# Performance work log

Hardware: AMD Instinct MI355X
Metric: run time of the kernel (lower is better)

## Reference

```python
import jax, jax.numpy as jnp
import numpy as np
import math

N, C_S, C_Z, C_IPA, H, NQ, NV = 768, 384, 128, 16, 12, 4, 8


def setup_inputs() -> dict:
    key = jax.random.key(0)
    ks = jax.random.split(key, 16)
    inp = {
        "s": jax.random.normal(ks[0], (N, C_S), jnp.float32),
        "z": jax.random.normal(ks[1], (N, N, C_Z), jnp.float32),
        "rots": jax.random.normal(ks[2], (N, 3, 3), jnp.float32),
        "trans": jax.random.normal(ks[3], (N, 3), jnp.float32),
        "mask": jnp.ones((N,), jnp.float32),
    }
    sc = 0.02
    inp["Wq"] = jax.random.normal(ks[4], (C_S, H * C_IPA), jnp.float32) * sc
    inp["bq"] = jnp.zeros((H * C_IPA,), jnp.float32)
    inp["Wkv"] = jax.random.normal(ks[5], (C_S, H * 2 * C_IPA), jnp.float32) * sc
    inp["bkv"] = jnp.zeros((H * 2 * C_IPA,), jnp.float32)
    inp["Wq3"] = jax.random.normal(ks[6], (C_S, H * 3 * NQ), jnp.float32) * sc
    inp["bq3"] = jnp.zeros((H * 3 * NQ,), jnp.float32)
    inp["Wkv3"] = jax.random.normal(ks[7], (C_S, H * 3 * (NQ + NV)), jnp.float32) * sc
    inp["bkv3"] = jnp.zeros((H * 3 * (NQ + NV),), jnp.float32)
    inp["Wb"] = jax.random.normal(ks[8], (C_Z, H), jnp.float32) * sc
    inp["bb"] = jnp.zeros((H,), jnp.float32)
    inp["hw"] = jnp.zeros((H,), jnp.float32)
    inp["Wo"] = jax.random.normal(ks[9], (H * (C_Z + C_IPA + NV * 4), C_S), jnp.float32) * sc
    inp["bo"] = jnp.zeros((C_S,), jnp.float32)
    return inp


def reference(s, z, rots, trans, mask, Wq, bq, Wkv, bkv, Wq3, bq3, Wkv3, bkv3, Wb, bb, hw, Wo, bo):
    normsize = math.sqrt(1.0 / (3 * C_IPA))
    normsize_B = math.sqrt(1.0 / 3.0)
    normsize_hw = math.sqrt(1.0 / (3 * NQ * 9.0 / 2))

    # scalar Q/K/V: [N, H, C_IPA]
    Q = (s @ Wq + bq).reshape(N, H, C_IPA)
    KV = (s @ Wkv + bkv).reshape(N, H, 2, C_IPA)
    K, V = KV[..., 0, :], KV[..., 1, :]

    # query points: project, place into global frame via rigid transform
    Q3 = (s @ Wq3 + bq3).reshape(N, 3, NQ * H).swapaxes(-1, -2)        # [N, NQ*H, 3]
    Q3 = jnp.einsum('nij,nkj->nki', rots, Q3) + trans[:, None, :]
    Q3 = Q3.reshape(N, H, NQ, 3)

    KV3 = (s @ Wkv3 + bkv3).reshape(N, 3, H * (NQ + NV)).swapaxes(-1, -2)
    KV3 = jnp.einsum('nij,nkj->nki', rots, KV3) + trans[:, None, :]
    KV3 = KV3.reshape(N, H, NQ + NV, 3)
    K3, V3 = KV3[:, :, :NQ, :], KV3[:, :, NQ:, :]                      # points per head

    # pair bias [N, N, H]
    B = z @ Wb + bb

    # scalar attention logits + pair bias
    AT = jnp.einsum('ihc,jhc->ijh', Q, K) * normsize + B * normsize_B

    # point attention: squared distances [N, N, H, NQ]
    d2 = jnp.sum(jnp.square(Q3[:, None] - K3[None, :]), axis=-1)
    hw_sp = jax.nn.softplus(hw) * normsize_hw                          # [H]
    AT3 = -0.5 * jnp.sum(d2 * hw_sp[None, None, :, None], axis=-1)     # [N, N, H]

    # mask bias: large negative where either residue masked out
    mask2 = mask[:, None] * mask[None, :]
    B3 = (mask2 - 1.0) * 1e9                                           # [N, N]

    AT = jax.nn.softmax(AT + AT3 + B3[..., None], axis=-2)             # softmax over j

    # scalar value aggregation
    O = jnp.einsum('ijh,jhc->ihc', AT, V).reshape(N, -1)

    # point value aggregation, then map back to local frame (inverse transform)
    O3 = jnp.einsum('ijh,jhcd->ihcd', AT, V3).reshape(N, H * NV, 3)
    O3 = jnp.einsum('nji,nkj->nki', rots, O3 - trans[:, None, :])      # rots^T @ (O3 - t)
    O3_norm = jnp.sqrt(jnp.sum(jnp.square(O3), axis=-1) + 1e-20)       # [N, H*NV]

    # pair representation aggregation
    O_pair = jnp.einsum('ijh,ijc->ihc', AT, z).reshape(N, -1)

    O_final = jnp.concatenate((O, O3[..., 0], O3[..., 1], O3[..., 2], O3_norm, O_pair), axis=-1)
    return O_final @ Wo + bo
```

## Files before the change

kernel.cpp:

```cpp
#include <hip/hip_runtime.h>
#include <cstdint>


typedef __attribute__((ext_vector_type(8))) short short8;
typedef __attribute__((ext_vector_type(4))) short short4_t;
typedef __attribute__((ext_vector_type(4))) float f32x4;

__device__ __forceinline__ unsigned short f2bf(float f) {
    unsigned u = __float_as_uint(f);
    u = (u + 0x7FFFu + ((u >> 16) & 1u)) >> 16;
    return (unsigned short)u;
}
__device__ __forceinline__ float bf2f(unsigned short s) {
    return __uint_as_float(((unsigned)s) << 16);
}
__device__ __forceinline__ unsigned pk2(float lo, float hi) {
    return (unsigned)f2bf(lo) | ((unsigned)f2bf(hi) << 16);
}
__device__ __forceinline__ int HOFF(int gg) {
    return gg * 6 + ((gg & 2) << 2);
}

__global__ __launch_bounds__(256) void proj_kernel(
    const float* __restrict__ s,
    const float* __restrict__ Wq,   const float* __restrict__ bq,
    const float* __restrict__ Wkv,  const float* __restrict__ bkv,
    const float* __restrict__ Wq3,  const float* __restrict__ bq3,
    const float* __restrict__ Wkv3, const float* __restrict__ bkv3,
    float* __restrict__ Qw, unsigned short* __restrict__ Kw,
    unsigned short* __restrict__ Vw,
    float* __restrict__ P3q, float* __restrict__ P3kv)
{
    __shared__ __align__(16) float s_lds[32 * 384];
    const int t  = threadIdx.x;
    const int r0 = blockIdx.x * 32;
    const int c0 = blockIdx.y * 128;

    for (int u = t; u < 3072; u += 256) {
        int r = u / 96, c4 = u - r * 96;
        *(float4*)&s_lds[r * 384 + c4 * 4] =
            *(const float4*)&s[(size_t)(r0 + r) * 384 + c4 * 4];
    }
    __syncthreads();

    const int rg = t >> 6;
    const int lc = t & 63;
    const int colA = c0 + lc;
    const int colB = c0 + lc + 64;

    const float *wpA, *wpB; int ldA, ldB; float biasA, biasB;
    {
        int col = colA;
        if (col < 192)      { wpA = Wq   + col;       ldA = 192; biasA = bq[col]; }
        else if (col < 576) { wpA = Wkv  + (col-192); ldA = 384; biasA = bkv[col-192]; }
        else if (col < 720) { wpA = Wq3  + (col-576); ldA = 144; biasA = bq3[col-576]; }
        else                { wpA = Wkv3 + (col-720); ldA = 432; biasA = bkv3[col-720]; }
        col = colB;
        if (col < 192)      { wpB = Wq   + col;       ldB = 192; biasB = bq[col]; }
        else if (col < 576) { wpB = Wkv  + (col-192); ldB = 384; biasB = bkv[col-192]; }
        else if (col < 720) { wpB = Wq3  + (col-576); ldB = 144; biasB = bq3[col-576]; }
        else                { wpB = Wkv3 + (col-720); ldB = 432; biasB = bkv3[col-720]; }
    }

    float acc0[8] = {}, acc1[8] = {};
    for (int k = 0; k < 384; k += 4) {
        float4 sv[8];
        #pragma unroll
        for (int r = 0; r < 8; r++)
            sv[r] = *(const float4*)&s_lds[(rg*8 + r) * 384 + k];
        #pragma unroll
        for (int kk = 0; kk < 4; kk++) {
            float w0 = wpA[(k + kk) * ldA];
            float w1 = wpB[(k + kk) * ldB];
            #pragma unroll
            for (int r = 0; r < 8; r++) {
                float sval = ((const float*)&sv[r])[kk];
                acc0[r] += sval * w0;
                acc1[r] += sval * w1;
            }
        }
    }

    #pragma unroll
    for (int q = 0; q < 2; q++) {
        int col   = q ? colB : colA;
        float bia = q ? biasB : biasA;
        #pragma unroll
        for (int r = 0; r < 8; r++) {
            int row = r0 + rg*8 + r;
            float v = (q ? acc1[r] : acc0[r]) + bia;
            if (col < 192) {
                Qw[(size_t)row*192 + col] = v;
            } else if (col < 576) {
                int c = col - 192, h = c >> 5, sub = c & 31;
                if (sub < 16) Kw[(size_t)row*192 + h*16 + sub]      = f2bf(v);
                else          Vw[(size_t)row*192 + h*16 + (sub-16)] = f2bf(v);
            } else if (col < 720) {
                P3q[(size_t)row*144 + (col-576)] = v;
            } else {
                P3kv[(size_t)row*432 + (col-720)] = v;
            }
        }
    }
}

__global__ __launch_bounds__(192) void rot3_kernel(
    const float* __restrict__ P3q, const float* __restrict__ P3kv,
    const float* __restrict__ rots, const float* __restrict__ trans,
    float* __restrict__ Q3w, unsigned short* __restrict__ K3w,
    unsigned short* __restrict__ V3w)
{
    const int n = blockIdx.x;
    const int t = threadIdx.x;
    float R[9];
    #pragma unroll
    for (int u = 0; u < 9; u++) R[u] = rots[n*9 + u];
    float T0 = trans[n*3+0], T1 = trans[n*3+1], T2 = trans[n*3+2];

    float p0, p1, p2;
    if (t < 48) {
        p0 = P3q[(size_t)n*144 + t];
        p1 = P3q[(size_t)n*144 + 48 + t];
        p2 = P3q[(size_t)n*144 + 96 + t];
    } else {
        int k = t - 48;
        p0 = P3kv[(size_t)n*432 + k];
        p1 = P3kv[(size_t)n*432 + 144 + k];
        p2 = P3kv[(size_t)n*432 + 288 + k];
    }
    float o0 = R[0]*p0 + R[1]*p1 + R[2]*p2 + T0;
    float o1 = R[3]*p0 + R[4]*p1 + R[5]*p2 + T1;
    float o2 = R[6]*p0 + R[7]*p1 + R[8]*p2 + T2;

    if (t < 48) {
        Q3w[(size_t)n*144 + t*3 + 0] = o0;
        Q3w[(size_t)n*144 + t*3 + 1] = o1;
        Q3w[(size_t)n*144 + t*3 + 2] = o2;
    } else {
        int k = t - 48, h = k / 12, m = k % 12;
        if (m < 4) {
            size_t base = (size_t)n*144 + (h*4 + m)*3;
            K3w[base+0] = f2bf(o0); K3w[base+1] = f2bf(o1); K3w[base+2] = f2bf(o2);
        } else {
            size_t base = (size_t)n*384 + (h*8 + (m-4))*4;
            V3w[base+0] = f2bf(o0); V3w[base+1] = f2bf(o1); V3w[base+2] = f2bf(o2);
        }
    }
}

__global__ __launch_bounds__(256, 4) void ipa_main(
    const float* __restrict__ z, const float* __restrict__ mask,
    const float* __restrict__ Wb, const float* __restrict__ bb,
    const float* __restrict__ hw,
    const float* __restrict__ Qw, const unsigned short* __restrict__ Kw,
    const unsigned short* __restrict__ Vw,
    const float* __restrict__ Q3w, const unsigned short* __restrict__ K3w,
    const unsigned short* __restrict__ V3w,
    float* __restrict__ part3)
{
    __shared__ __align__(16) unsigned short z_l[90 * 88];
    __shared__ __align__(16) unsigned short wbT_l[16 * 136];
    __shared__ __align__(16) float          p_l[32 * 17];
    __shared__ __align__(16) unsigned short pT_l[16 * 40];
    __shared__ __align__(16) float          Q_lds[192];
    __shared__ __align__(16) float          Q3_lds[144];
    __shared__ float hw_lds[12], bb_lds[12];

    const int i     = blockIdx.x >> 1;
    const int chunk = blockIdx.x & 1;
    const int t    = threadIdx.x;
    const int lane = t & 63;
    const int wv   = t >> 6;
    const int g    = lane >> 4;
    const int lm   = lane & 15;

    if (t < 192) Q_lds[t]  = Qw[(size_t)i*192 + t];
    if (t < 144) Q3_lds[t] = Q3w[(size_t)i*144 + t];
    if (t < 12) {
        hw_lds[t] = log1pf(__expf(hw[t])) * 0.13608276348795434f;
        bb_lds[t] = bb[t];
    }
    if (t < 160) pT_l[480 + t] = 0;
    for (int u = t; u < 1536; u += 256) {
        int h = u % 12, c = u / 12;
        wbT_l[h*136 + c] = f2bf(Wb[c*12 + h]);
    }
    const float mask_i = mask[i];

    f32x4 opA = {0,0,0,0}, opB = {0,0,0,0};
    float oacc = 0.0f;
    float o3x = 0, o3y = 0, o3z = 0;
    float dena = 0;
    const int oh = t >> 4, oc = t & 15;
    int o3h = -1, o3v = 0, o3j0 = 0, o3j1 = 32, o3slot = 0;
    if (t >= 192)    { o3h = (t - 192) >> 3;      o3v = (t - 192) & 7; }
    else if (t < 32) { o3h = 8 + (t >> 3);        o3v = t & 7;        o3j1 = 16; }
    else if (t < 64) { o3h = 8 + ((t - 32) >> 3); o3v = (t - 32) & 7; o3j0 = 16; o3slot = 1; }
    const int denh = (t >= 64 && t < 76) ? (t - 64) : -1;

    const int jj  = t >> 3, c16 = t & 7;
    const float* zbase = z + ((size_t)i*768 + chunk*384 + jj)*128 + c16*16;
    const int chS  = (jj >> 2)*8 + c16;
    const int chP  = chS + HOFF(chS >> 4);
    const int sidx = chP*88 + (jj & 3)*16;

    __syncthreads();

    for (int tile = 0; tile < 12; tile++) {
        const int j0 = chunk*384 + tile*32;

        {
            const float* zp = zbase + (size_t)tile * 32 * 128;
            float4 f0 = *(const float4*)(zp + 0);
            float4 f1 = *(const float4*)(zp + 4);
            float4 f2 = *(const float4*)(zp + 8);
            float4 f3 = *(const float4*)(zp + 12);
            uint4* dst = (uint4*)&z_l[sidx];
            dst[0] = uint4{pk2(f0.x,f0.y), pk2(f0.z,f0.w), pk2(f1.x,f1.y), pk2(f1.z,f1.w)};
            dst[1] = uint4{pk2(f2.x,f2.y), pk2(f2.z,f2.w), pk2(f3.x,f3.y), pk2(f3.z,f3.w)};
        }
        __syncthreads();

        if (wv < 2) {
            f32x4 ab = {0,0,0,0};
            const int jt = wv;
            #pragma unroll
            for (int ks = 0; ks < 4; ks++) {
                short8 bf = *(const short8*)&wbT_l[lm*136 + ks*32 + g*8];
                int jr = jt*16 + lm;
                int ch = (jr >> 2)*8 + ks*2 + (g >> 1);
                int cp = ch + HOFF(ch >> 4);
                short8 a = *(const short8*)&z_l[cp*88 + (jr & 3)*16 + (g & 1)*8];
                ab = __builtin_amdgcn_mfma_f32_16x16x32_bf16(a, bf, ab, 0, 0, 0);
            }
            if (lm < 12) {
                #pragma unroll
                for (int r = 0; r < 4; r++)
                    p_l[(jt*16 + g*4 + r)*17 + lm] = ab[r];
            }
        }
        __syncthreads();

        #pragma unroll
        for (int rep = 0; rep < 2; rep++) {
            int pr = t + rep*256;
            if (pr < 384) {
                int jjq = pr / 12;
                int h   = pr - jjq*12;
                int j   = j0 + jjq;
                float Bv = p_l[jjq*17 + h];
                const unsigned short* kp = Kw + (size_t)j*192 + h*16;
                short8 kA = *(const short8*)(kp);
                short8 kB = *(const short8*)(kp + 8);
                float qk = 0.0f;
                #pragma unroll
                for (int e = 0; e < 8; e++) qk += Q_lds[h*16 + e]     * bf2f((unsigned short)kA[e]);
                #pragma unroll
                for (int e = 0; e < 8; e++) qk += Q_lds[h*16 + 8 + e] * bf2f((unsigned short)kB[e]);
                const unsigned short* k3p = K3w + (size_t)j*144 + h*12;
                short4_t c0v = *(const short4_t*)(k3p);
                short4_t c1v = *(const short4_t*)(k3p + 4);
                short4_t c2v = *(const short4_t*)(k3p + 8);
                float d2 = 0.0f;
                #pragma unroll
                for (int e = 0; e < 4; e++) { float d = Q3_lds[h*12 + e]     - bf2f((unsigned short)c0v[e]); d2 += d*d; }
                #pragma unroll
                for (int e = 0; e < 4; e++) { float d = Q3_lds[h*12 + 4 + e] - bf2f((unsigned short)c1v[e]); d2 += d*d; }
                #pragma unroll
                for (int e = 0; e < 4; e++) { float d = Q3_lds[h*12 + 8 + e] - bf2f((unsigned short)c2v[e]); d2 += d*d; }
                float mj = mask[j];
                float lg = qk * 0.14433756729740643f
                         + (Bv + bb_lds[h]) * 0.5773502691896258f
                         - 0.5f * hw_lds[h] * d2
                         + (mask_i * mj - 1.0f) * 1e9f;
                float p = __expf(lg);
                p_l[jjq*17 + h]  = p;
                pT_l[h*40 + jjq] = f2bf(p);
            }
        }
        __syncthreads();

        {
            const int nt0 = wv*2;
            short8 ap = *(const short8*)((const char*)pT_l + lm*80 + g*16);
            short8 b0, b1;
            #pragma unroll
            for (int e = 0; e < 8; e++) {
                int jje = g*8 + e;
                int su  = (jje >> 2)*8;
                int ro  = (jje & 3)*16;
                int cp0 = su + nt0 + HOFF(g);
                b0[e] = (short)z_l[cp0*88 + ro + lm];
                b1[e] = (short)z_l[(cp0 + 1)*88 + ro + lm];
            }
            opA = __builtin_amdgcn_mfma_f32_16x16x32_bf16(ap, b0, opA, 0, 0, 0);
            opB = __builtin_amdgcn_mfma_f32_16x16x32_bf16(ap, b1, opB, 0, 0, 0);
        }
        if (t < 192) {
            #pragma unroll 8
            for (int jjq = 0; jjq < 32; jjq++) {
                float p = p_l[jjq*17 + oh];
                oacc += p * bf2f(Vw[(size_t)(j0 + jjq)*192 + oh*16 + oc]);
            }
        }
        if (o3h >= 0) {
            #pragma unroll 8
            for (int jjq = o3j0; jjq < o3j1; jjq++) {
                float p = p_l[jjq*17 + o3h];
                short4_t v4 = *(const short4_t*)(V3w + (size_t)(j0 + jjq)*384 + (o3h*8 + o3v)*4);
                o3x += p * bf2f((unsigned short)v4[0]);
                o3y += p * bf2f((unsigned short)v4[1]);
                o3z += p * bf2f((unsigned short)v4[2]);
            }
        }
        if (denh >= 0) {
            #pragma unroll 8
            for (int jjq = 0; jjq < 32; jjq++) dena += p_l[jjq*17 + denh];
        }
        __syncthreads();
    }

    float* pb = part3 + (size_t)blockIdx.x * 2560;
    if (t < 192) pb[t] = oacc;
    if (o3h >= 0) {
        int base = 192 + o3slot*288 + (o3h*8 + o3v)*3;
        pb[base+0] = o3x; pb[base+1] = o3y; pb[base+2] = o3z;
    }
    if (denh >= 0) pb[2304 + denh] = dena;
    {
        const int nt0 = wv*2;
        #pragma unroll
        for (int r = 0; r < 4; r++) {
            int h = g*4 + r;
            if (h < 12) {
                pb[768 + h*128 + nt0*16 + lm]       = opA[r];
                pb[768 + h*128 + (nt0 + 1)*16 + lm] = opB[r];
            }
        }
    }
}

__global__ __launch_bounds__(256) void combine_kernel(
    const float* __restrict__ part3, const float* __restrict__ rots,
    const float* __restrict__ trans, unsigned short* __restrict__ OF)
{
    const int i = blockIdx.x;
    const int t = threadIdx.x;
    const float* pa = part3 + (size_t)i*2*2560;
    const float* pb = pa + 2560;
    __shared__ float den_s[12];
    if (t < 12) den_s[t] = pa[2304 + t] + pb[2304 + t];
    __syncthreads();

    const size_t ofb = (size_t)i * 2112;
    if (t < 192) OF[ofb + t] = f2bf((pa[t] + pb[t]) / den_s[t >> 4]);
    if (t < 96) {
        int h = t >> 3, v = t & 7;
        float den = den_s[h];
        int base = 192 + t*3;
        float m0 = pa[base+0] + pb[base+0];
        float m1 = pa[base+1] + pb[base+1];
        float m2 = pa[base+2] + pb[base+2];
        if (h >= 8) {
            m0 += pa[base+288+0] + pb[base+288+0];
            m1 += pa[base+288+1] + pb[base+288+1];
            m2 += pa[base+288+2] + pb[base+288+2];
        }
        m0 = m0 / den - trans[i*3+0];
        m1 = m1 / den - trans[i*3+1];
        m2 = m2 / den - trans[i*3+2];
        const float* R = rots + (size_t)i*9;
        float r0v = R[0]*m0 + R[3]*m1 + R[6]*m2;
        float r1v = R[1]*m0 + R[4]*m1 + R[7]*m2;
        float r2v = R[2]*m0 + R[5]*m1 + R[8]*m2;
        float nrm = sqrtf(r0v*r0v + r1v*r1v + r2v*r2v + 1e-20f);
        int hv = h*8 + v;
        OF[ofb + 192 + hv] = f2bf(r0v);
        OF[ofb + 288 + hv] = f2bf(r1v);
        OF[ofb + 384 + hv] = f2bf(r2v);
        OF[ofb + 480 + hv] = f2bf(nrm);
    }
    for (int u = t; u < 1536; u += 256) {
        OF[ofb + 576 + u] = f2bf((pa[768 + u] + pb[768 + u]) / den_s[u >> 7]);
    }
}

__global__ __launch_bounds__(256) void wot_kernel(
    const float* __restrict__ Wo, unsigned short* __restrict__ WoT)
{
    int id = blockIdx.x * 256 + threadIdx.x;
    int c  = id % 384;
    int k8 = id / 384;
    unsigned short tmp[8];
    #pragma unroll
    for (int e = 0; e < 8; e++)
        tmp[e] = f2bf(Wo[(size_t)(k8*8 + e)*384 + c]);
    uint4 o;
    o.x = (unsigned)tmp[0] | ((unsigned)tmp[1] << 16);
    o.y = (unsigned)tmp[2] | ((unsigned)tmp[3] << 16);
    o.z = (unsigned)tmp[4] | ((unsigned)tmp[5] << 16);
    o.w = (unsigned)tmp[6] | ((unsigned)tmp[7] << 16);
    *(uint4*)&WoT[(size_t)c*2112 + k8*8] = o;
}

__global__ __launch_bounds__(256) void out_gemm2(
    const unsigned short* __restrict__ OF, const unsigned short* __restrict__ WoT,
    const float* __restrict__ bo, float* __restrict__ out)
{
    const int t = threadIdx.x;
    const int wv = t >> 6, lane = t & 63, g = lane >> 4, lm = lane & 15;
    const int i0 = blockIdx.x * 32;
    const int c0 = blockIdx.y * 128 + wv * 32;

    f32x4 acc00 = {0,0,0,0}, acc01 = {0,0,0,0};
    f32x4 acc10 = {0,0,0,0}, acc11 = {0,0,0,0};

    const unsigned short* a0p = OF  + (size_t)(i0 + lm)*2112      + g*8;
    const unsigned short* a1p = OF  + (size_t)(i0 + 16 + lm)*2112 + g*8;
    const unsigned short* b0p = WoT + (size_t)(c0 + lm)*2112      + g*8;
    const unsigned short* b1p = WoT + (size_t)(c0 + 16 + lm)*2112 + g*8;

    #pragma unroll 2
    for (int k = 0; k < 2112; k += 32) {
        short8 a0 = *(const short8*)(a0p + k);
        short8 a1 = *(const short8*)(a1p + k);
        short8 b0 = *(const short8*)(b0p + k);
        short8 b1 = *(const short8*)(b1p + k);
        acc00 = __builtin_amdgcn_mfma_f32_16x16x32_bf16(a0, b0, acc00, 0, 0, 0);
        acc01 = __builtin_amdgcn_mfma_f32_16x16x32_bf16(a0, b1, acc01, 0, 0, 0);
        acc10 = __builtin_amdgcn_mfma_f32_16x16x32_bf16(a1, b0, acc10, 0, 0, 0);
        acc11 = __builtin_amdgcn_mfma_f32_16x16x32_bf16(a1, b1, acc11, 0, 0, 0);
    }

    const int colA = c0 + lm, colB = c0 + 16 + lm;
    const float bA = bo[colA], bB = bo[colB];
    #pragma unroll
    for (int r = 0; r < 4; r++) {
        int rowA = i0 + g*4 + r;
        int rowB = i0 + 16 + g*4 + r;
        out[(size_t)rowA*384 + colA] = acc00[r] + bA;
        out[(size_t)rowA*384 + colB] = acc01[r] + bB;
        out[(size_t)rowB*384 + colA] = acc10[r] + bA;
        out[(size_t)rowB*384 + colB] = acc11[r] + bB;
    }
}

extern "C" void kernel_launch(void* const* d_in, const int* in_sizes, int n_in,
                              void* d_out, int out_size, void* d_ws, size_t ws_size,
                              hipStream_t stream) {
    const float* s     = (const float*)d_in[0];
    const float* z     = (const float*)d_in[1];
    const float* rots  = (const float*)d_in[2];
    const float* trans = (const float*)d_in[3];
    const float* mask  = (const float*)d_in[4];
    const float* Wq    = (const float*)d_in[5];
    const float* bq    = (const float*)d_in[6];
    const float* Wkv   = (const float*)d_in[7];
    const float* bkv   = (const float*)d_in[8];
    const float* Wq3   = (const float*)d_in[9];
    const float* bq3   = (const float*)d_in[10];
    const float* Wkv3  = (const float*)d_in[11];
    const float* bkv3  = (const float*)d_in[12];
    const float* Wb    = (const float*)d_in[13];
    const float* bb    = (const float*)d_in[14];
    const float* hw    = (const float*)d_in[15];
    const float* Wo    = (const float*)d_in[16];
    const float* bo    = (const float*)d_in[17];
    float* out = (float*)d_out;

    char* ws = (char*)d_ws;
    float*          Qw   = (float*)(ws + 0);
    float*          Q3w  = (float*)(ws + 589824);
    unsigned short* Kw   = (unsigned short*)(ws + 1032192);
    unsigned short* Vw   = (unsigned short*)(ws + 1327104);
    unsigned short* K3w  = (unsigned short*)(ws + 1622016);
    unsigned short* V3w  = (unsigned short*)(ws + 1843200);
    float*          P3q  = (float*)(ws + 2433024);
    float*          P3kv = (float*)(ws + 2875392);
    unsigned short* OF   = (unsigned short*)(ws + 4202496);
    float*          part3 = (float*)(ws + 7446528);
    unsigned short* WoT  = (unsigned short*)(ws + 23175168);

    wot_kernel<<<396, 256, 0, stream>>>(Wo, WoT);
    proj_kernel<<<dim3(24, 9), 256, 0, stream>>>(
        s, Wq, bq, Wkv, bkv, Wq3, bq3, Wkv3, bkv3, Qw, Kw, Vw, P3q, P3kv);
    rot3_kernel<<<768, 192, 0, stream>>>(P3q, P3kv, rots, trans, Q3w, K3w, V3w);
    ipa_main<<<1536, 256, 0, stream>>>(
        z, mask, Wb, bb, hw, Qw, Kw, Vw, Q3w, K3w, V3w, part3);
    combine_kernel<<<768, 256, 0, stream>>>(part3, rots, trans, OF);
    out_gemm2<<<dim3(24, 3), 256, 0, stream>>>(OF, WoT, bo, out);
}
```

Before: 270.0 us.

## Stage output GEMM tiles in LDS and pad Q tables against bank conflicts

The output GEMM now loads 32x64 and 128x64 tiles of OF and WoT into shared memory once per block and shares them across waves. Previously each wave read its own A and B fragments straight from global memory, so the OF rows were fetched redundantly by all four waves. In the main attention kernel, the Q and Q3 LDS tables get padded strides of 17 and 13 to cut bank conflicts. The two-pass logit loop is rewritten as a lambda whose second pass runs only for threads 128 and up. The GEMM adds two barriers per k-step and gives up the previous direct-load pipelining.

```diff
diff --git a/kernel.cpp b/kernel.cpp
--- a/kernel.cpp
+++ b/kernel.cpp
@@ -162,8 +162,8 @@
     __shared__ __align__(16) unsigned short wbT_l[16 * 136];
     __shared__ __align__(16) float          p_l[32 * 17];
     __shared__ __align__(16) unsigned short pT_l[16 * 40];
-    __shared__ __align__(16) float          Q_lds[192];
-    __shared__ __align__(16) float          Q3_lds[144];
+    __shared__ __align__(16) float          Q_lds[12 * 17];
+    __shared__ __align__(16) float          Q3_lds[12 * 13];
     __shared__ float hw_lds[12], bb_lds[12];
 
     const int i     = blockIdx.x >> 1;
@@ -174,8 +174,8 @@
     const int g    = lane >> 4;
     const int lm   = lane & 15;
 
-    if (t < 192) Q_lds[t]  = Qw[(size_t)i*192 + t];
-    if (t < 144) Q3_lds[t] = Q3w[(size_t)i*144 + t];
+    if (t < 192) Q_lds[(t >> 4)*17 + (t & 15)] = Qw[(size_t)i*192 + t];
+    if (t < 144) Q3_lds[(t / 12)*13 + (t % 12)] = Q3w[(size_t)i*144 + t];
     if (t < 12) {
         hw_lds[t] = log1pf(__expf(hw[t])) * 0.13608276348795434f;
         bb_lds[t] = bb[t];
@@ -241,10 +241,8 @@
         }
         __syncthreads();
 
-        #pragma unroll
-        for (int rep = 0; rep < 2; rep++) {
-            int pr = t + rep*256;
-            if (pr < 384) {
+        {
+            auto b2item = [&](int pr) {
                 int jjq = pr / 12;
                 int h   = pr - jjq*12;
                 int j   = j0 + jjq;
@@ -254,20 +252,20 @@
                 short8 kB = *(const short8*)(kp + 8);
                 float qk = 0.0f;
                 #pragma unroll
-                for (int e = 0; e < 8; e++) qk += Q_lds[h*16 + e]     * bf2f((unsigned short)kA[e]);
+                for (int e = 0; e < 8; e++) qk += Q_lds[h*17 + e]     * bf2f((unsigned short)kA[e]);
                 #pragma unroll
-                for (int e = 0; e < 8; e++) qk += Q_lds[h*16 + 8 + e] * bf2f((unsigned short)kB[e]);
+                for (int e = 0; e < 8; e++) qk += Q_lds[h*17 + 8 + e] * bf2f((unsigned short)kB[e]);
                 const unsigned short* k3p = K3w + (size_t)j*144 + h*12;
                 short4_t c0v = *(const short4_t*)(k3p);
                 short4_t c1v = *(const short4_t*)(k3p + 4);
                 short4_t c2v = *(const short4_t*)(k3p + 8);
                 float d2 = 0.0f;
                 #pragma unroll
-                for (int e = 0; e < 4; e++) { float d = Q3_lds[h*12 + e]     - bf2f((unsigned short)c0v[e]); d2 += d*d; }
+                for (int e = 0; e < 4; e++) { float d = Q3_lds[h*13 + e]     - bf2f((unsigned short)c0v[e]); d2 += d*d; }
                 #pragma unroll
-                for (int e = 0; e < 4; e++) { float d = Q3_lds[h*12 + 4 + e] - bf2f((unsigned short)c1v[e]); d2 += d*d; }
+                for (int e = 0; e < 4; e++) { float d = Q3_lds[h*13 + 4 + e] - bf2f((unsigned short)c1v[e]); d2 += d*d; }
                 #pragma unroll
-                for (int e = 0; e < 4; e++) { float d = Q3_lds[h*12 + 8 + e] - bf2f((unsigned short)c2v[e]); d2 += d*d; }
+                for (int e = 0; e < 4; e++) { float d = Q3_lds[h*13 + 8 + e] - bf2f((unsigned short)c2v[e]); d2 += d*d; }
                 float mj = mask[j];
                 float lg = qk * 0.14433756729740643f
                          + (Bv + bb_lds[h]) * 0.5773502691896258f
@@ -276,7 +274,9 @@
                 float p = __expf(lg);
                 p_l[jjq*17 + h]  = p;
                 pT_l[h*40 + jjq] = f2bf(p);
-            }
+            };
+            b2item(t);
+            if (t >= 128) b2item(t + 128);
         }
         __syncthreads();
 
@@ -407,37 +407,48 @@
     const unsigned short* __restrict__ OF, const unsigned short* __restrict__ WoT,
     const float* __restrict__ bo, float* __restrict__ out)
 {
+    __shared__ __align__(16) unsigned short aT[32 * 72];
+    __shared__ __align__(16) unsigned short bT[128 * 72];
     const int t = threadIdx.x;
     const int wv = t >> 6, lane = t & 63, g = lane >> 4, lm = lane & 15;
     const int i0 = blockIdx.x * 32;
-    const int c0 = blockIdx.y * 128 + wv * 32;
+    const int c0 = blockIdx.y * 128;
 
     f32x4 acc00 = {0,0,0,0}, acc01 = {0,0,0,0};
     f32x4 acc10 = {0,0,0,0}, acc11 = {0,0,0,0};
 
-    const unsigned short* a0p = OF  + (size_t)(i0 + lm)*2112      + g*8;
-    const unsigned short* a1p = OF  + (size_t)(i0 + 16 + lm)*2112 + g*8;
-    const unsigned short* b0p = WoT + (size_t)(c0 + lm)*2112      + g*8;
-    const unsigned short* b1p = WoT + (size_t)(c0 + 16 + lm)*2112 + g*8;
-
-    #pragma unroll 2
-    for (int k = 0; k < 2112; k += 32) {
-        short8 a0 = *(const short8*)(a0p + k);
-        short8 a1 = *(const short8*)(a1p + k);
-        short8 b0 = *(const short8*)(b0p + k);
-        short8 b1 = *(const short8*)(b1p + k);
-        acc00 = __builtin_amdgcn_mfma_f32_16x16x32_bf16(a0, b0, acc00, 0, 0, 0);
-        acc01 = __builtin_amdgcn_mfma_f32_16x16x32_bf16(a0, b1, acc01, 0, 0, 0);
-        acc10 = __builtin_amdgcn_mfma_f32_16x16x32_bf16(a1, b0, acc10, 0, 0, 0);
-        acc11 = __builtin_amdgcn_mfma_f32_16x16x32_bf16(a1, b1, acc11, 0, 0, 0);
-    }
-
-    const int colA = c0 + lm, colB = c0 + 16 + lm;
+    const int sr = t >> 3, sc = (t & 7) * 8;
+
+    for (int k0 = 0; k0 < 2112; k0 += 64) {
+        __syncthreads();
+        *(uint4*)&aT[sr*72 + sc] =
+            *(const uint4*)&OF[(size_t)(i0 + sr)*2112 + k0 + sc];
+        #pragma unroll
+        for (int q = 0; q < 4; q++) {
+            int br = q*32 + sr;
+            *(uint4*)&bT[br*72 + sc] =
+                *(const uint4*)&WoT[(size_t)(c0 + br)*2112 + k0 + sc];
+        }
+        __syncthreads();
+        #pragma unroll
+        for (int kk = 0; kk < 2; kk++) {
+            short8 a0 = *(const short8*)&aT[lm*72        + kk*32 + g*8];
+            short8 a1 = *(const short8*)&aT[(16+lm)*72   + kk*32 + g*8];
+            short8 b0 = *(const short8*)&bT[(wv*32+lm)*72    + kk*32 + g*8];
+            short8 b1 = *(const short8*)&bT[(wv*32+16+lm)*72 + kk*32 + g*8];
+            acc00 = __builtin_amdgcn_mfma_f32_16x16x32_bf16(a0, b0, acc00, 0, 0, 0);
+            acc01 = __builtin_amdgcn_mfma_f32_16x16x32_bf16(a0, b1, acc01, 0, 0, 0);
+            acc10 = __builtin_amdgcn_mfma_f32_16x16x32_bf16(a1, b0, acc10, 0, 0, 0);
+            acc11 = __builtin_amdgcn_mfma_f32_16x16x32_bf16(a1, b1, acc11, 0, 0, 0);
+        }
+    }
+
+    const int colA = c0 + wv*32 + lm, colB = colA + 16;
     const float bA = bo[colA], bB = bo[colB];
     #pragma unroll
     for (int r = 0; r < 4; r++) {
         int rowA = i0 + g*4 + r;
-        int rowB = i0 + 16 + g*4 + r;
+        int rowB = rowA + 16;
         out[(size_t)rowA*384 + colA] = acc00[r] + bA;
         out[(size_t)rowA*384 + colB] = acc01[r] + bB;
         out[(size_t)rowB*384 + colA] = acc10[r] + bA;
```

Result: faster. 264.1 us (-2.2%).
